# Performance work log

Measured on AMD Instinct MI355X. Metric: run time of the kernel, lower is better.

The kernel has to match this reference:

```python
import jax, jax.numpy as jnp
import numpy as np

B, S, D, H, HD, F = 2, 2048, 2048, 16, 128, 8192
EPS = 1e-5
THETA = 10000.0
NEG = -1e30


def _rmsnorm(x, w):
    v = jnp.mean(jnp.square(x.astype(jnp.float32)), axis=-1, keepdims=True)
    return (x.astype(jnp.float32) * jax.lax.rsqrt(v + EPS)).astype(x.dtype) * w


def _rope(x):
    # x: [B, S, H, HD]; llama-style rotate-half rotary embedding
    inv_freq = 1.0 / (THETA ** (jnp.arange(0, HD, 2, dtype=jnp.float32) / HD))
    ang = jnp.arange(S, dtype=jnp.float32)[:, None] * inv_freq[None, :]  # [S, HD//2]
    cos = jnp.concatenate([jnp.cos(ang), jnp.cos(ang)], axis=-1)[None, :, None, :]
    sin = jnp.concatenate([jnp.sin(ang), jnp.sin(ang)], axis=-1)[None, :, None, :]
    x1, x2 = jnp.split(x, 2, axis=-1)
    return x * cos + jnp.concatenate([-x2, x1], axis=-1) * sin


def _mlp(x, wg, wu, wd):
    # SiLU-gated HiggsAudioMLP: down(silu(gate(x)) * up(x))
    return (jax.nn.silu(x @ wg) * (x @ wu)) @ wd


def setup_inputs() -> dict:
    key = jax.random.key(0)
    ks = jax.random.split(key, 12)
    std = 0.02
    p = lambda k, shape: jax.random.normal(k, shape, dtype=jnp.float32) * std
    return {
        "hidden_states": jax.random.normal(ks[0], (B, S, D), dtype=jnp.float32),
        "audio_out_mask": jax.random.randint(ks[1], (B, S), 0, 2).astype(bool),
        "wq": p(ks[2], (D, H * HD)),
        "wk": p(ks[3], (D, H * HD)),
        "wv": p(ks[4], (D, H * HD)),
        "wo": p(ks[5], (H * HD, D)),
        "input_ln_w": jnp.ones((D,), jnp.float32),
        "post_ln_w": jnp.ones((D,), jnp.float32),
        "audio_post_ln_w": jnp.ones((D,), jnp.float32),
        "w_gate_t": p(ks[6], (D, F)),
        "w_up_t": p(ks[7], (D, F)),
        "w_down_t": p(ks[8], (F, D)),
        "w_gate_a": p(ks[9], (D, F)),
        "w_up_a": p(ks[10], (D, F)),
        "w_down_a": p(ks[11], (F, D)),
    }


def reference(hidden_states, audio_out_mask, wq, wk, wv, wo, input_ln_w, post_ln_w,
              audio_post_ln_w, w_gate_t, w_up_t, w_down_t, w_gate_a, w_up_a, w_down_a):
    # ---- self-attention block ----
    residual = hidden_states
    h = _rmsnorm(hidden_states, input_ln_w)
    q = _rope((h @ wq).reshape(B, S, H, HD))
    k = _rope((h @ wk).reshape(B, S, H, HD))
    v = (h @ wv).reshape(B, S, H, HD)
    scores = jnp.einsum("bqhd,bkhd->bhqk", q, k) / float(np.sqrt(HD))
    causal = jnp.tril(jnp.ones((S, S), bool))
    scores = jnp.where(causal[None, None], scores, NEG)
    attn = jax.nn.softmax(scores, axis=-1)
    ctx = jnp.einsum("bhqk,bkhd->bqhd", attn, v).reshape(B, S, H * HD)
    hidden_states = residual + ctx @ wo
    # ---- dual FFN, per-token routed by audio_out_mask ----
    residual = hidden_states
    text_out = _mlp(_rmsnorm(hidden_states, post_ln_w), w_gate_t, w_up_t, w_down_t)
    audio_out = _mlp(_rmsnorm(hidden_states, audio_post_ln_w), w_gate_a, w_up_a, w_down_a)
    return residual + jnp.where(audio_out_mask[..., None], audio_out, text_out)
```

## Files before the change

### kernel.cpp

```cpp
#include <hip/hip_runtime.h>


#define BB 2
#define SS 2048
#define DD 2048
#define HH 16
#define HDD 128
#define FF 8192
#define TT (BB*SS)
#define RPAD 4608

typedef unsigned short ushort_t;
typedef __bf16 bf16x8 __attribute__((ext_vector_type(8)));
typedef float f32x4 __attribute__((ext_vector_type(4)));

#define DEV static __device__ __forceinline__

DEV float bf2f(ushort_t u) { __bf16 b; __builtin_memcpy(&b, &u, 2); return (float)b; }
DEV ushort_t f2bf(float f) { __bf16 b = (__bf16)f; ushort_t u; __builtin_memcpy(&u, &b, 2); return u; }

DEV void gl_lds16(const ushort_t* g, ushort_t* l) {
    __builtin_amdgcn_global_load_lds((const __attribute__((address_space(1))) void*)g,
                                     (__attribute__((address_space(3))) void*)l, 16, 0, 0);
}

#define BARRIER() do { asm volatile("" ::: "memory"); __builtin_amdgcn_s_barrier(); asm volatile("" ::: "memory"); } while (0)
#define LGKM0()   asm volatile("s_waitcnt lgkmcnt(0)" ::: "memory")

__global__ __launch_bounds__(256) void partition_k(const unsigned char* __restrict__ raw,
                                                   int* __restrict__ perm,
                                                   int* __restrict__ header) {
    __shared__ int flag;
    __shared__ int ct[256], ca[256], st[256], sa[256];
    __shared__ int Nt_s, Na_s;
    const int tid = threadIdx.x;
    if (tid == 0) flag = 0;
    __syncthreads();
    int any = 0;
    for (int i = tid; i < TT; i += 256)
        if ((i & 3) != 0 && raw[i] != 0) any = 1;
    if (any) atomicOr(&flag, 1);
    __syncthreads();
    const int is_byte = flag;
    auto mget = [&](int r) -> int {
        return is_byte ? (raw[r] != 0) : (((const int*)raw)[r] != 0);
    };
    int c0 = 0, c1 = 0;
#pragma unroll
    for (int i = 0; i < 16; ++i) {
        if (mget(tid * 16 + i)) c1++; else c0++;
    }
    ct[tid] = c0; ca[tid] = c1;
    __syncthreads();
    if (tid == 0) {
        int at = 0, aa = 0;
        for (int i = 0; i < 256; ++i) {
            st[i] = at; at += ct[i];
            sa[i] = aa; aa += ca[i];
        }
        Nt_s = at; Na_s = aa;
    }
    __syncthreads();
    const int Nt = Nt_s, Na = Na_s;
    const int A0 = (Nt + 255) & ~255;
    const int live = A0 + ((Na + 255) & ~255);
    int pt = st[tid], pa = A0 + sa[tid];
#pragma unroll
    for (int i = 0; i < 16; ++i) {
        const int r = tid * 16 + i;
        if (mget(r)) perm[pa++] = r; else perm[pt++] = r;
    }
    for (int i = Nt + tid; i < A0; i += 256) perm[i] = -1;
    for (int i = A0 + Na + tid; i < RPAD; i += 256) perm[i] = -1;
    if (tid == 0) { header[0] = Nt; header[1] = A0; header[2] = Na; header[3] = live; }
}

struct ConvSeg { const float* in; ushort_t* out; int K, N, cumEnd; };
struct ConvArgs { ConvSeg s[10]; };

__global__ __launch_bounds__(256) void convw_all(ConvArgs a) {
    __shared__ float t[32][33];
    int bid = blockIdx.x;
    int i = 0;
    while (bid >= a.s[i].cumEnd) ++i;
    const int base = (i == 0) ? 0 : a.s[i - 1].cumEnd;
    const int local = bid - base;
    const float* __restrict__ in = a.s[i].in;
    ushort_t* __restrict__ out = a.s[i].out;
    const int K = a.s[i].K, N = a.s[i].N;
    const int ntile = N >> 5;
    const int n0 = (local % ntile) * 32, k0 = (local / ntile) * 32;
    const int tx = threadIdx.x & 31, ty = threadIdx.x >> 5;
#pragma unroll
    for (int j = 0; j < 4; ++j)
        t[ty + 8 * j][tx] = in[(size_t)(k0 + ty + 8 * j) * N + n0 + tx];
    __syncthreads();
#pragma unroll
    for (int j = 0; j < 4; ++j)
        out[(size_t)(n0 + ty + 8 * j) * K + k0 + tx] = f2bf(t[tx][ty + 8 * j]);
}

__global__ __launch_bounds__(256) void rmsnorm_k(const float* __restrict__ x,
                                                 const float* __restrict__ wt,
                                                 ushort_t* __restrict__ out) {
    const int row = blockIdx.x, tid = threadIdx.x;
    const float4* xr = (const float4*)(x + (size_t)row * DD);
    float4 v0 = xr[tid * 2], v1 = xr[tid * 2 + 1];
    float ss = v0.x * v0.x + v0.y * v0.y + v0.z * v0.z + v0.w * v0.w
             + v1.x * v1.x + v1.y * v1.y + v1.z * v1.z + v1.w * v1.w;
#pragma unroll
    for (int d = 1; d < 64; d <<= 1) ss += __shfl_xor(ss, d);
    __shared__ float red[4];
    if ((tid & 63) == 0) red[tid >> 6] = ss;
    __syncthreads();
    const float tot = red[0] + red[1] + red[2] + red[3];
    const float sc = rsqrtf(tot * (1.0f / DD) + 1e-5f);
    const float4* wr = (const float4*)wt;
    float4 w0 = wr[tid * 2], w1 = wr[tid * 2 + 1];
    ushort_t* o = out + (size_t)row * DD + tid * 8;
    o[0] = f2bf(v0.x * sc * w0.x); o[1] = f2bf(v0.y * sc * w0.y);
    o[2] = f2bf(v0.z * sc * w0.z); o[3] = f2bf(v0.w * sc * w0.w);
    o[4] = f2bf(v1.x * sc * w1.x); o[5] = f2bf(v1.y * sc * w1.y);
    o[6] = f2bf(v1.z * sc * w1.z); o[7] = f2bf(v1.w * sc * w1.w);
}

__global__ __launch_bounds__(256) void rmsnorm_gather(const float* __restrict__ x,
                                                      const float* __restrict__ wt_text,
                                                      const float* __restrict__ wt_audio,
                                                      const int* __restrict__ perm,
                                                      const int* __restrict__ header,
                                                      ushort_t* __restrict__ out) {
    const int i = blockIdx.x, tid = threadIdx.x;
    const int p = perm[i];
    ushort_t* o = out + (size_t)i * DD + tid * 8;
    if (p < 0) {
#pragma unroll
        for (int j = 0; j < 8; ++j) o[j] = 0;
        return;
    }
    const float* wt = (i < header[1]) ? wt_text : wt_audio;
    const float4* xr = (const float4*)(x + (size_t)p * DD);
    float4 v0 = xr[tid * 2], v1 = xr[tid * 2 + 1];
    float ss = v0.x * v0.x + v0.y * v0.y + v0.z * v0.z + v0.w * v0.w
             + v1.x * v1.x + v1.y * v1.y + v1.z * v1.z + v1.w * v1.w;
#pragma unroll
    for (int d = 1; d < 64; d <<= 1) ss += __shfl_xor(ss, d);
    __shared__ float red[4];
    if ((tid & 63) == 0) red[tid >> 6] = ss;
    __syncthreads();
    const float tot = red[0] + red[1] + red[2] + red[3];
    const float sc = rsqrtf(tot * (1.0f / DD) + 1e-5f);
    const float4* wr = (const float4*)wt;
    float4 w0 = wr[tid * 2], w1 = wr[tid * 2 + 1];
    o[0] = f2bf(v0.x * sc * w0.x); o[1] = f2bf(v0.y * sc * w0.y);
    o[2] = f2bf(v0.z * sc * w0.z); o[3] = f2bf(v0.w * sc * w0.w);
    o[4] = f2bf(v1.x * sc * w1.x); o[5] = f2bf(v1.y * sc * w1.y);
    o[6] = f2bf(v1.z * sc * w1.z); o[7] = f2bf(v1.w * sc * w1.w);
}

__global__ __launch_bounds__(256) void rope_tab(float* __restrict__ cosb,
                                                float* __restrict__ sinb) {
    const int idx = blockIdx.x * 256 + threadIdx.x;
    const int s = idx >> 6, i = idx & 63;
    const float inv = powf(10000.0f, -(float)i * (1.0f / 64.0f));
    const float ang = (float)s * inv;
    cosb[idx] = cosf(ang);
    sinb[idx] = sinf(ang);
}

__global__ __launch_bounds__(256) void rope_qk(ushort_t* __restrict__ qb,
                                               ushort_t* __restrict__ kb,
                                               const float* __restrict__ cosb,
                                               const float* __restrict__ sinb) {
    const int gid = blockIdx.x * 256 + threadIdx.x;
    ushort_t* x = (gid < TT * 1024) ? qb : kb;
    const int g = gid & (TT * 1024 - 1);
    const int row = g >> 10, p = g & 1023;
    const int h = p >> 6, d = p & 63;
    const int s = row & (SS - 1);
    const size_t base = (size_t)row * DD + h * HDD + d;
    const float x1 = bf2f(x[base]), x2 = bf2f(x[base + 64]);
    const float c = cosb[s * 64 + d], sn = sinb[s * 64 + d];
    x[base]      = f2bf(x1 * c - x2 * sn);
    x[base + 64] = f2bf(x2 * c + x1 * sn);
}

__global__ __launch_bounds__(256, 2) void gemm_qkv(
    const ushort_t* __restrict__ A, const ushort_t* __restrict__ W,
    ushort_t* __restrict__ qb, ushort_t* __restrict__ kb, ushort_t* __restrict__ vt) {
    __shared__ ushort_t As[128 * 32];
    __shared__ ushort_t Bs[128 * 32];
    const int tid = threadIdx.x;
    const int w = tid >> 6, lane = tid & 63;
    const int bx = blockIdx.x;
    const int kind = bx >> 4;
    const int n0 = (bx & 15) * 128;
    const int m0 = blockIdx.y * 128;
    const int wr = w >> 1, wc = w & 1;
    f32x4 acc[4][4] = {};
    const ushort_t* gA = A + (size_t)m0 * DD;
    const ushort_t* gB = W + (size_t)kind * DD * DD + (size_t)n0 * DD;
    const int c0 = tid, c1 = 256 + tid;
    const int r0 = c0 >> 2, o0 = (c0 & 3) * 8;
    const int r1 = c1 >> 2, o1 = (c1 & 3) * 8;
    ushort_t* lA0 = &As[(w * 64) * 8];
    ushort_t* lA1 = &As[(256 + w * 64) * 8];
    ushort_t* lB0 = &Bs[(w * 64) * 8];
    ushort_t* lB1 = &Bs[(256 + w * 64) * 8];
    for (int k0 = 0; k0 < DD; k0 += 32) {
        __syncthreads();
        gl_lds16(gA + (size_t)r0 * DD + k0 + o0, lA0);
        gl_lds16(gA + (size_t)r1 * DD + k0 + o1, lA1);
        gl_lds16(gB + (size_t)r0 * DD + k0 + o0, lB0);
        gl_lds16(gB + (size_t)r1 * DD + k0 + o1, lB1);
        asm volatile("s_waitcnt vmcnt(0)" ::: "memory");
        __syncthreads();
        const int ko = (lane >> 4) * 8;
        const int ra = wr * 64 + (lane & 15);
        const int rb = wc * 64 + (lane & 15);
        bf16x8 af[4], bfv[4];
#pragma unroll
        for (int mi = 0; mi < 4; ++mi) af[mi] = *(const bf16x8*)&As[(ra + mi * 16) * 32 + ko];
#pragma unroll
        for (int ni = 0; ni < 4; ++ni) bfv[ni] = *(const bf16x8*)&Bs[(rb + ni * 16) * 32 + ko];
#pragma unroll
        for (int mi = 0; mi < 4; ++mi)
#pragma unroll
            for (int ni = 0; ni < 4; ++ni)
                acc[mi][ni] = __builtin_amdgcn_mfma_f32_16x16x32_bf16(af[mi], bfv[ni], acc[mi][ni], 0, 0, 0);
    }
    const int cl = lane & 15, r4 = (lane >> 4) * 4;
#pragma unroll
    for (int mi = 0; mi < 4; ++mi)
#pragma unroll
        for (int ni = 0; ni < 4; ++ni)
#pragma unroll
            for (int j = 0; j < 4; ++j) {
                const int r = m0 + wr * 64 + mi * 16 + r4 + j;
                const int c = n0 + wc * 64 + ni * 16 + cl;
                const ushort_t v = f2bf(acc[mi][ni][j]);
                if (kind == 0) {
                    qb[(size_t)r * DD + c] = v;
                } else if (kind == 1) {
                    kb[(size_t)r * DD + c] = v;
                } else {
                    const int b = r >> 11, s = r & (SS - 1), h = c >> 7, d = c & 127;
                    vt[(((size_t)(b * HH + h) * HDD + d) << 11) + s] = v;
                }
            }
}

__global__ __launch_bounds__(256, 2) void gemm_wo(
    const ushort_t* __restrict__ A, const ushort_t* __restrict__ Bt,
    float* __restrict__ C, const float* __restrict__ resid) {
    __shared__ ushort_t As[128 * 32];
    __shared__ ushort_t Bs[128 * 32];
    const int tid = threadIdx.x;
    const int w = tid >> 6, lane = tid & 63;
    const int m0 = blockIdx.y * 128, n0 = blockIdx.x * 128;
    const int wr = w >> 1, wc = w & 1;
    f32x4 acc[4][4] = {};
    const ushort_t* gA = A + (size_t)m0 * DD;
    const ushort_t* gB = Bt + (size_t)n0 * DD;
    const int c0 = tid, c1 = 256 + tid;
    const int r0 = c0 >> 2, o0 = (c0 & 3) * 8;
    const int r1 = c1 >> 2, o1 = (c1 & 3) * 8;
    ushort_t* lA0 = &As[(w * 64) * 8];
    ushort_t* lA1 = &As[(256 + w * 64) * 8];
    ushort_t* lB0 = &Bs[(w * 64) * 8];
    ushort_t* lB1 = &Bs[(256 + w * 64) * 8];
    for (int k0 = 0; k0 < DD; k0 += 32) {
        __syncthreads();
        gl_lds16(gA + (size_t)r0 * DD + k0 + o0, lA0);
        gl_lds16(gA + (size_t)r1 * DD + k0 + o1, lA1);
        gl_lds16(gB + (size_t)r0 * DD + k0 + o0, lB0);
        gl_lds16(gB + (size_t)r1 * DD + k0 + o1, lB1);
        asm volatile("s_waitcnt vmcnt(0)" ::: "memory");
        __syncthreads();
        const int ko = (lane >> 4) * 8;
        const int ra = wr * 64 + (lane & 15);
        const int rb = wc * 64 + (lane & 15);
        bf16x8 af[4], bfv[4];
#pragma unroll
        for (int mi = 0; mi < 4; ++mi) af[mi] = *(const bf16x8*)&As[(ra + mi * 16) * 32 + ko];
#pragma unroll
        for (int ni = 0; ni < 4; ++ni) bfv[ni] = *(const bf16x8*)&Bs[(rb + ni * 16) * 32 + ko];
#pragma unroll
        for (int mi = 0; mi < 4; ++mi)
#pragma unroll
            for (int ni = 0; ni < 4; ++ni)
                acc[mi][ni] = __builtin_amdgcn_mfma_f32_16x16x32_bf16(af[mi], bfv[ni], acc[mi][ni], 0, 0, 0);
    }
    const int cl = lane & 15, r4 = (lane >> 4) * 4;
#pragma unroll
    for (int mi = 0; mi < 4; ++mi)
#pragma unroll
        for (int ni = 0; ni < 4; ++ni)
#pragma unroll
            for (int j = 0; j < 4; ++j) {
                const int r = m0 + wr * 64 + mi * 16 + r4 + j;
                const int c = n0 + wc * 64 + ni * 16 + cl;
                const size_t idx = (size_t)r * DD + c;
                C[idx] = resid[idx] + acc[mi][ni][j];
            }
}

__global__ __launch_bounds__(256, 2) void gemm_down_c(
    const ushort_t* __restrict__ A, const ushort_t* __restrict__ Bt_text,
    const ushort_t* __restrict__ Bt_audio, float* __restrict__ C,
    const int* __restrict__ perm, const int* __restrict__ header) {
    const int m0 = blockIdx.y * 128;
    if (m0 >= header[3]) return;
    const ushort_t* Bt = (m0 >= header[1]) ? Bt_audio : Bt_text;
    __shared__ ushort_t As[128 * 32];
    __shared__ ushort_t Bs[128 * 32];
    const int tid = threadIdx.x;
    const int w = tid >> 6, lane = tid & 63;
    const int n0 = blockIdx.x * 128;
    const int wr = w >> 1, wc = w & 1;
    f32x4 acc[4][4] = {};
    const ushort_t* gA = A + (size_t)m0 * FF;
    const ushort_t* gB = Bt + (size_t)n0 * FF;
    const int c0 = tid, c1 = 256 + tid;
    const int r0 = c0 >> 2, o0 = (c0 & 3) * 8;
    const int r1 = c1 >> 2, o1 = (c1 & 3) * 8;
    ushort_t* lA0 = &As[(w * 64) * 8];
    ushort_t* lA1 = &As[(256 + w * 64) * 8];
    ushort_t* lB0 = &Bs[(w * 64) * 8];
    ushort_t* lB1 = &Bs[(256 + w * 64) * 8];
    for (int k0 = 0; k0 < FF; k0 += 32) {
        __syncthreads();
        gl_lds16(gA + (size_t)r0 * FF + k0 + o0, lA0);
        gl_lds16(gA + (size_t)r1 * FF + k0 + o1, lA1);
        gl_lds16(gB + (size_t)r0 * FF + k0 + o0, lB0);
        gl_lds16(gB + (size_t)r1 * FF + k0 + o1, lB1);
        asm volatile("s_waitcnt vmcnt(0)" ::: "memory");
        __syncthreads();
        const int ko = (lane >> 4) * 8;
        const int ra = wr * 64 + (lane & 15);
        const int rb = wc * 64 + (lane & 15);
        bf16x8 af[4], bfv[4];
#pragma unroll
        for (int mi = 0; mi < 4; ++mi) af[mi] = *(const bf16x8*)&As[(ra + mi * 16) * 32 + ko];
#pragma unroll
        for (int ni = 0; ni < 4; ++ni) bfv[ni] = *(const bf16x8*)&Bs[(rb + ni * 16) * 32 + ko];
#pragma unroll
        for (int mi = 0; mi < 4; ++mi)
#pragma unroll
            for (int ni = 0; ni < 4; ++ni)
                acc[mi][ni] = __builtin_amdgcn_mfma_f32_16x16x32_bf16(af[mi], bfv[ni], acc[mi][ni], 0, 0, 0);
    }
    const int cl = lane & 15, r4 = (lane >> 4) * 4;
#pragma unroll
    for (int mi = 0; mi < 4; ++mi)
#pragma unroll
        for (int ni = 0; ni < 4; ++ni)
#pragma unroll
            for (int j = 0; j < 4; ++j) {
                const int r = m0 + wr * 64 + mi * 16 + r4 + j;
                const int p = perm[r];
                if (p >= 0) {
                    const int c = n0 + wc * 64 + ni * 16 + cl;
                    float* q = C + (size_t)p * DD + c;
                    *q = *q + acc[mi][ni][j];
                }
            }
}

__global__ __launch_bounds__(512, 2) void gemm_gu8(
    const ushort_t* __restrict__ A,
    const ushort_t* __restrict__ Bg_t, const ushort_t* __restrict__ Bu_t,
    const ushort_t* __restrict__ Bg_a, const ushort_t* __restrict__ Bu_a,
    ushort_t* __restrict__ act, const int* __restrict__ header) {
    const int nwg = gridDim.x * gridDim.y;
    int bid = blockIdx.y * gridDim.x + blockIdx.x;
    bid = (bid & 7) * (nwg >> 3) + (bid >> 3);
    const int bx = bid % 64;
    const int by = bid / 64;
    const int m0 = by * 256;
    if (m0 >= header[3]) return;
    const bool audio = (m0 >= header[1]);
    const ushort_t* Bg = audio ? Bg_a : Bg_t;
    const ushort_t* Bu = audio ? Bu_a : Bu_t;
    const int n0g = bx * 128;

    __shared__ ushort_t smem[65536];
    const int tid = threadIdx.x;
    const int w = tid >> 6, lane = tid & 63;
    const int wm = w >> 2, wn = w & 3;
    const int f16 = lane & 15, g4 = lane >> 4;

    const int rl = tid >> 3;
    const int cc8 = (((tid & 7) ^ ((tid >> 3) & 7)) * 8);
    const int wchunk = w * 64;

    const ushort_t* gA = A + (size_t)m0 * DD;

    auto stageA_h = [&](int buf, int k0, int h) {
#pragma unroll
        for (int j = 0; j < 2; ++j) {
            const int r = h * 128 + j * 64 + rl;
            gl_lds16(gA + (size_t)r * DD + k0 + cc8,
                     &smem[buf * 32768 + h * 8192 + (j * 512 + wchunk) * 8]);
        }
    };
    auto stageB_h = [&](int buf, int k0, int h) {
#pragma unroll
        for (int j = 0; j < 2; ++j) {
            const int br = h * 128 + j * 64 + rl;
            const int ty = (br >> 4) & 1;
            const int grow = ((br >> 5) << 4) + (br & 15);
            const ushort_t* src = (ty ? Bu : Bg) + (size_t)(n0g + grow) * DD + k0 + cc8;
            gl_lds16(src, &smem[buf * 32768 + 16384 + h * 8192 + (j * 512 + wchunk) * 8]);
        }
    };

    const int aBase = (wm * 128 + f16) * 64;
    const int bBase = (wn * 64 + f16) * 64;
    int cswz[2];
    cswz[0] = ((g4 ^ (f16 & 7)) * 8);
    cswz[1] = (((4 + g4) ^ (f16 & 7)) * 8);

    f32x4 acc[8][4] = {};
    bf16x8 af[4][2], b0[2][2], b1[2][2];

    stageA_h(0, 0, 0); stageA_h(0, 0, 1);
    stageB_h(0, 0, 0); stageB_h(0, 0, 1);
    stageA_h(1, 64, 0); stageB_h(1, 64, 0);
    asm volatile("s_waitcnt vmcnt(4)" ::: "memory");
    BARRIER();

    const int nt = DD / 64;
    for (int t = 0; t < nt; ++t) {
        const int buf = t & 1, obuf = buf ^ 1;
        const int ab = buf * 32768, bb = buf * 32768 + 16384;
        const int k1 = (t + 1) * 64, k2 = (t + 2) * 64;
        const bool pf1 = (t + 1) < nt, pf2 = (t + 2) < nt;
#pragma unroll
        for (int m = 0; m < 4; ++m)
#pragma unroll
            for (int ks = 0; ks < 2; ++ks)
                af[m][ks] = *(const bf16x8*)&smem[ab + aBase + m * 1024 + cswz[ks]];
#pragma unroll
        for (int n = 0; n < 2; ++n)
#pragma unroll
            for (int ks = 0; ks < 2; ++ks)
                b0[n][ks] = *(const bf16x8*)&smem[bb + bBase + n * 1024 + cswz[ks]];
        if (pf1) stageA_h(obuf, k1, 1);
        BARRIER();
        LGKM0();
        __builtin_amdgcn_s_setprio(1);
#pragma unroll
        for (int m = 0; m < 4; ++m)
#pragma unroll
            for (int n = 0; n < 2; ++n)
#pragma unroll
                for (int ks = 0; ks < 2; ++ks)
                    acc[m][n] = __builtin_amdgcn_mfma_f32_16x16x32_bf16(af[m][ks], b0[n][ks], acc[m][n], 0, 0, 0);
        __builtin_amdgcn_s_setprio(0);
        BARRIER();
#pragma unroll
        for (int n = 0; n < 2; ++n)
#pragma unroll
            for (int ks = 0; ks < 2; ++ks)
                b1[n][ks] = *(const bf16x8*)&smem[bb + bBase + (2 + n) * 1024 + cswz[ks]];
        if (pf1) stageB_h(obuf, k1, 1);
        BARRIER();
        LGKM0();
        __builtin_amdgcn_s_setprio(1);
#pragma unroll
        for (int m = 0; m < 4; ++m)
#pragma unroll
            for (int n = 0; n < 2; ++n)
#pragma unroll
                for (int ks = 0; ks < 2; ++ks)
                    acc[m][2 + n] = __builtin_amdgcn_mfma_f32_16x16x32_bf16(af[m][ks], b1[n][ks], acc[m][2 + n], 0, 0, 0);
        __builtin_amdgcn_s_setprio(0);
        BARRIER();
#pragma unroll
        for (int m = 0; m < 4; ++m)
#pragma unroll
            for (int ks = 0; ks < 2; ++ks)
                af[m][ks] = *(const bf16x8*)&smem[ab + aBase + (4 + m) * 1024 + cswz[ks]];
        BARRIER();
        LGKM0();
        __builtin_amdgcn_s_setprio(1);
#pragma unroll
        for (int m = 0; m < 4; ++m)
#pragma unroll
            for (int n = 0; n < 2; ++n)
#pragma unroll
                for (int ks = 0; ks < 2; ++ks)
                    acc[4 + m][n] = __builtin_amdgcn_mfma_f32_16x16x32_bf16(af[m][ks], b0[n][ks], acc[4 + m][n], 0, 0, 0);
        __builtin_amdgcn_s_setprio(0);
        BARRIER();
        if (pf2) { stageA_h(buf, k2, 0); stageB_h(buf, k2, 0); }
        BARRIER();
        __builtin_amdgcn_s_setprio(1);
#pragma unroll
        for (int m = 0; m < 4; ++m)
#pragma unroll
            for (int n = 0; n < 2; ++n)
#pragma unroll
                for (int ks = 0; ks < 2; ++ks)
                    acc[4 + m][2 + n] = __builtin_amdgcn_mfma_f32_16x16x32_bf16(af[m][ks], b1[n][ks], acc[4 + m][2 + n], 0, 0, 0);
        __builtin_amdgcn_s_setprio(0);
        if (pf2)      { asm volatile("s_waitcnt vmcnt(4)" ::: "memory"); }
        else if (pf1) { asm volatile("s_waitcnt vmcnt(0)" ::: "memory"); }
        BARRIER();
    }

    const int r4 = g4 * 4;
#pragma unroll
    for (int m = 0; m < 8; ++m)
#pragma unroll
        for (int np = 0; np < 2; ++np) {
            const int f = n0g + (wn * 2 + np) * 16 + f16;
#pragma unroll
            for (int j = 0; j < 4; ++j) {
                const int r = m0 + wm * 128 + m * 16 + r4 + j;
                const float g = acc[m][np * 2][j], u = acc[m][np * 2 + 1][j];
                act[(size_t)r * FF + f] = f2bf(g / (1.0f + __expf(-g)) * u);
            }
        }
}

__global__ __launch_bounds__(512, 2) void attn_k(
    const ushort_t* __restrict__ qb, const ushort_t* __restrict__ kb,
    const ushort_t* __restrict__ vt, ushort_t* __restrict__ ctx) {
    __shared__ ushort_t Ks[2][64 * 128];
    __shared__ ushort_t Vs[2][128 * 64];
    __shared__ ushort_t Pw[8][16 * 64];
    const int tid = threadIdx.x, w = tid >> 6, lane = tid & 63;
    const int qt = gridDim.x - 1 - blockIdx.x;
    const int bh = blockIdx.y, b = bh >> 4, h = bh & 15;
    const int q0 = qt * 128 + w * 16;
    const int f16 = lane & 15, g4 = lane >> 4;
    bf16x8 aq[4];
    {
        const ushort_t* qr = qb + ((size_t)(b * SS + q0 + f16)) * DD + h * HDD + g4 * 8;
#pragma unroll
        for (int ko = 0; ko < 4; ++ko) aq[ko] = *(const bf16x8*)(qr + ko * 32);
    }
    auto stageKV = [&](int bufi, int kt) {
        const int sk0 = kt * 64;
#pragma unroll
        for (int i = 0; i < 2; ++i) {
            const int c = i * 512 + tid;
            const int csrc = ((c & 15) ^ ((c >> 4) & 7)) * 8;
            gl_lds16(kb + ((size_t)(b * SS + sk0 + (c >> 4))) * DD + h * HDD + csrc,
                     &Ks[bufi][(i * 512 + w * 64) * 8]);
        }
#pragma unroll
        for (int i = 0; i < 2; ++i) {
            const int c = i * 512 + tid;
            const int csrc = ((c & 7) ^ ((c >> 3) & 7)) * 8;
            gl_lds16(vt + ((size_t)((b * HH + h) * HDD + (c >> 3))) * SS + sk0 + csrc,
                     &Vs[bufi][(i * 512 + w * 64) * 8]);
        }
    };
    f32x4 o[8] = {};
    float mrow[4] = {-3e38f, -3e38f, -3e38f, -3e38f};
    float lrow[4] = {};
    const int nkv = 2 * qt + 2;
    stageKV(0, 0);
    for (int kt = 0; kt < nkv; ++kt) {
        const int cur = kt & 1;
        if (kt < nkv - 1) {
            stageKV(cur ^ 1, kt + 1);
            asm volatile("s_waitcnt vmcnt(4)" ::: "memory");
        } else {
            asm volatile("s_waitcnt vmcnt(0)" ::: "memory");
        }
        BARRIER();
        f32x4 s[4] = {};
#pragma unroll
        for (int ko = 0; ko < 4; ++ko)
#pragma unroll
            for (int ni = 0; ni < 4; ++ni) {
                bf16x8 bk = *(const bf16x8*)&Ks[cur][(ni * 16 + f16) * 128 + (((ko * 4 + g4) ^ (f16 & 7)) * 8)];
                s[ni] = __builtin_amdgcn_mfma_f32_16x16x32_bf16(aq[ko], bk, s[ni], 0, 0, 0);
            }
        const float scale = 0.08838834764831843f;
#pragma unroll
        for (int ni = 0; ni < 4; ++ni)
#pragma unroll
            for (int j = 0; j < 4; ++j) {
                float v = s[ni][j] * scale;
                const int kg = kt * 64 + ni * 16 + f16;
                const int qg = q0 + g4 * 4 + j;
                if (kg > qg) v = -1e30f;
                s[ni][j] = v;
            }
#pragma unroll
        for (int j = 0; j < 4; ++j) {
            float tm = fmaxf(fmaxf(s[0][j], s[1][j]), fmaxf(s[2][j], s[3][j]));
#pragma unroll
            for (int dd = 1; dd < 16; dd <<= 1) tm = fmaxf(tm, __shfl_xor(tm, dd));
            const float mn = fmaxf(mrow[j], tm);
            const float corr = __expf(mrow[j] - mn);
            float sum = 0.f;
#pragma unroll
            for (int ni = 0; ni < 4; ++ni) {
                const float p = __expf(s[ni][j] - mn);
                s[ni][j] = p;
                sum += p;
            }
#pragma unroll
            for (int dd = 1; dd < 16; dd <<= 1) sum += __shfl_xor(sum, dd);
            lrow[j] = lrow[j] * corr + sum;
            mrow[j] = mn;
#pragma unroll
            for (int di = 0; di < 8; ++di) o[di][j] *= corr;
        }
#pragma unroll
        for (int ni = 0; ni < 4; ++ni)
#pragma unroll
            for (int j = 0; j < 4; ++j) {
                const int prow = g4 * 4 + j;
                const int pcb = ni * 2 + (f16 >> 3);
                Pw[w][prow * 64 + ((pcb ^ (prow & 7)) * 8) + (f16 & 7)] = f2bf(s[ni][j]);
            }
#pragma unroll
        for (int ks = 0; ks < 2; ++ks) {
            bf16x8 pa = *(const bf16x8*)&Pw[w][f16 * 64 + (((ks * 4 + g4) ^ (f16 & 7)) * 8)];
#pragma unroll
            for (int di = 0; di < 8; ++di) {
                bf16x8 bv = *(const bf16x8*)&Vs[cur][(di * 16 + f16) * 64 + (((ks * 4 + g4) ^ (f16 & 7)) * 8)];
                o[di] = __builtin_amdgcn_mfma_f32_16x16x32_bf16(pa, bv, o[di], 0, 0, 0);
            }
        }
        BARRIER();
    }
    float inv[4];
#pragma unroll
    for (int j = 0; j < 4; ++j) inv[j] = 1.0f / lrow[j];
#pragma unroll
    for (int di = 0; di < 8; ++di)
#pragma unroll
        for (int j = 0; j < 4; ++j) {
            const int r = q0 + g4 * 4 + j;
            ctx[((size_t)(b * SS + r)) * DD + h * HDD + di * 16 + f16] = f2bf(o[di][j] * inv[j]);
        }
}

extern "C" void kernel_launch(void* const* d_in, const int* in_sizes, int n_in,
                              void* d_out, int out_size, void* d_ws, size_t ws_size,
                              hipStream_t stream) {
    (void)in_sizes; (void)n_in; (void)out_size; (void)ws_size;
    const float* hs  = (const float*)d_in[0];
    const unsigned char* mask_raw = (const unsigned char*)d_in[1];
    const float* wq  = (const float*)d_in[2];
    const float* wk  = (const float*)d_in[3];
    const float* wv  = (const float*)d_in[4];
    const float* wo  = (const float*)d_in[5];
    const float* iln = (const float*)d_in[6];
    const float* pln = (const float*)d_in[7];
    const float* aln = (const float*)d_in[8];
    const float* wgt = (const float*)d_in[9];
    const float* wut = (const float*)d_in[10];
    const float* wdt = (const float*)d_in[11];
    const float* wga = (const float*)d_in[12];
    const float* wua = (const float*)d_in[13];
    const float* wda = (const float*)d_in[14];

    const size_t SZ_W1 = (size_t)DD * DD * 2;
    const size_t SZ_W2 = (size_t)DD * FF * 2;
    const size_t SZ_A  = (size_t)TT * DD * 2;

    char* ws = (char*)d_ws;
    size_t off = 0;
    auto take = [&](size_t n) { char* p = ws + off; off += n; return p; };
    ushort_t* wq_t  = (ushort_t*)take(SZ_W1);
    ushort_t* wk_t  = (ushort_t*)take(SZ_W1);
    ushort_t* wv_t  = (ushort_t*)take(SZ_W1);
    ushort_t* wo_t  = (ushort_t*)take(SZ_W1);
    ushort_t* wg_tb = (ushort_t*)take(SZ_W2);
    ushort_t* wu_tb = (ushort_t*)take(SZ_W2);
    ushort_t* wd_tb = (ushort_t*)take(SZ_W2);
    ushort_t* wg_ab = (ushort_t*)take(SZ_W2);
    ushort_t* wu_ab = (ushort_t*)take(SZ_W2);
    ushort_t* wd_ab = (ushort_t*)take(SZ_W2);
    char* actreg = take(6 * SZ_A);
    float* cosb = (float*)take((size_t)SS * 64 * 4);
    float* sinb = (float*)take((size_t)SS * 64 * 4);
    int* perm   = (int*)take(RPAD * 4);
    int* header = (int*)take(64);

    ushort_t* h_bf = (ushort_t*)(actreg);
    ushort_t* qb   = (ushort_t*)(actreg + 1 * SZ_A);
    ushort_t* kb   = (ushort_t*)(actreg + 2 * SZ_A);
    ushort_t* vt   = (ushort_t*)(actreg + 3 * SZ_A);
    ushort_t* ctx  = (ushort_t*)(actreg + 4 * SZ_A);
    ushort_t* hn_c  = (ushort_t*)(actreg);
    ushort_t* act_c = (ushort_t*)(actreg + (size_t)RPAD * DD * 2);

    const dim3 blk(256);

    partition_k<<<1, blk, 0, stream>>>(mask_raw, perm, header);

    ConvArgs ca;
    int cum = 0;
    auto seg = [&](int i, const float* in, ushort_t* out, int K, int N) {
        cum += (N / 32) * (K / 32);
        ca.s[i] = ConvSeg{in, out, K, N, cum};
    };
    seg(0, wq, wq_t, DD, DD);
    seg(1, wk, wk_t, DD, DD);
    seg(2, wv, wv_t, DD, DD);
    seg(3, wo, wo_t, DD, DD);
    seg(4, wgt, wg_tb, DD, FF);
    seg(5, wut, wu_tb, DD, FF);
    seg(6, wdt, wd_tb, FF, DD);
    seg(7, wga, wg_ab, DD, FF);
    seg(8, wua, wu_ab, DD, FF);
    seg(9, wda, wd_ab, FF, DD);
    convw_all<<<cum, blk, 0, stream>>>(ca);

    rope_tab<<<(SS * 64) / 256, blk, 0, stream>>>(cosb, sinb);

    rmsnorm_k<<<TT, blk, 0, stream>>>(hs, iln, h_bf);
    gemm_qkv<<<dim3(48, TT / 128), blk, 0, stream>>>(h_bf, wq_t, qb, kb, vt);
    rope_qk<<<(2 * TT * 1024) / 256, blk, 0, stream>>>(qb, kb, cosb, sinb);
    attn_k<<<dim3(SS / 128, BB * HH), dim3(512), 0, stream>>>(qb, kb, vt, ctx);
    gemm_wo<<<dim3(DD / 128, TT / 128), blk, 0, stream>>>(ctx, wo_t, (float*)d_out, hs);

    rmsnorm_gather<<<RPAD, blk, 0, stream>>>((const float*)d_out, pln, aln, perm, header, hn_c);
    gemm_gu8<<<dim3(FF / 128, RPAD / 256), dim3(512), 0, stream>>>(hn_c, wg_tb, wu_tb, wg_ab, wu_ab, act_c, header);
    gemm_down_c<<<dim3(DD / 128, RPAD / 128), blk, 0, stream>>>(act_c, wd_tb, wd_ab, (float*)d_out, perm, header);
}
```

Baseline: 1.110 ms.

## Replace QKV and output GEMMs with pipelined 256x128 template kernel; lazy softmax rescale

Replaces the simple single-buffered gemm_qkv and gemm_wo kernels with one templated 512-thread kernel. It uses 256x128 tiles, K-step 64, a double-buffered LDS with XOR swizzle, staggered global-to-LDS loads overlapped with MFMA, s_setprio around the MFMA phases, and a block-id remap across XCDs. This targets the per-iteration full vmcnt(0) stalls and the low data reuse of the old kernels. Separately, the attention softmax now skips the running-max rescale of the output accumulators unless the new max exceeds the old one by more than 8 anywhere in the wave. That saves exp and multiply work, but lets exponentials grow up to e^8 before renormalising.

```diff
diff --git a/kernel.cpp b/kernel.cpp
--- a/kernel.cpp
+++ b/kernel.cpp
@@ -185,123 +185,140 @@
     x[base + 64] = f2bf(x2 * c + x1 * sn);
 }
 
-__global__ __launch_bounds__(256, 2) void gemm_qkv(
+template <int EPI>
+__global__ __launch_bounds__(512, 2) void gemm_nt8(
     const ushort_t* __restrict__ A, const ushort_t* __restrict__ W,
-    ushort_t* __restrict__ qb, ushort_t* __restrict__ kb, ushort_t* __restrict__ vt) {
-    __shared__ ushort_t As[128 * 32];
-    __shared__ ushort_t Bs[128 * 32];
+    int K, ushort_t* __restrict__ o0, ushort_t* __restrict__ o1,
+    ushort_t* __restrict__ o2, float* __restrict__ Cf,
+    const float* __restrict__ resid) {
+    const int nwg = gridDim.x * gridDim.y;
+    int bid = blockIdx.y * gridDim.x + blockIdx.x;
+    bid = (bid & 7) * (nwg >> 3) + (bid >> 3);
+    const int bxx = bid % gridDim.x;
+    const int byy = bid / gridDim.x;
+    const int m0 = byy * 256;
+    int kind = 0, n0;
+    const ushort_t* B;
+    if (EPI == 0) {
+        kind = bxx >> 4;
+        n0 = (bxx & 15) * 128;
+        B = W + (size_t)kind * DD * DD + (size_t)n0 * K;
+    } else {
+        n0 = bxx * 128;
+        B = W + (size_t)n0 * K;
+    }
+    __shared__ ushort_t smem[49152];
     const int tid = threadIdx.x;
     const int w = tid >> 6, lane = tid & 63;
-    const int bx = blockIdx.x;
-    const int kind = bx >> 4;
-    const int n0 = (bx & 15) * 128;
-    const int m0 = blockIdx.y * 128;
-    const int wr = w >> 1, wc = w & 1;
-    f32x4 acc[4][4] = {};
-    const ushort_t* gA = A + (size_t)m0 * DD;
-    const ushort_t* gB = W + (size_t)kind * DD * DD + (size_t)n0 * DD;
-    const int c0 = tid, c1 = 256 + tid;
-    const int r0 = c0 >> 2, o0 = (c0 & 3) * 8;
-    const int r1 = c1 >> 2, o1 = (c1 & 3) * 8;
-    ushort_t* lA0 = &As[(w * 64) * 8];
-    ushort_t* lA1 = &As[(256 + w * 64) * 8];
-    ushort_t* lB0 = &Bs[(w * 64) * 8];
-    ushort_t* lB1 = &Bs[(256 + w * 64) * 8];
-    for (int k0 = 0; k0 < DD; k0 += 32) {
-        __syncthreads();
-        gl_lds16(gA + (size_t)r0 * DD + k0 + o0, lA0);
-        gl_lds16(gA + (size_t)r1 * DD + k0 + o1, lA1);
-        gl_lds16(gB + (size_t)r0 * DD + k0 + o0, lB0);
-        gl_lds16(gB + (size_t)r1 * DD + k0 + o1, lB1);
-        asm volatile("s_waitcnt vmcnt(0)" ::: "memory");
-        __syncthreads();
-        const int ko = (lane >> 4) * 8;
-        const int ra = wr * 64 + (lane & 15);
-        const int rb = wc * 64 + (lane & 15);
-        bf16x8 af[4], bfv[4];
-#pragma unroll
-        for (int mi = 0; mi < 4; ++mi) af[mi] = *(const bf16x8*)&As[(ra + mi * 16) * 32 + ko];
-#pragma unroll
-        for (int ni = 0; ni < 4; ++ni) bfv[ni] = *(const bf16x8*)&Bs[(rb + ni * 16) * 32 + ko];
-#pragma unroll
-        for (int mi = 0; mi < 4; ++mi)
-#pragma unroll
-            for (int ni = 0; ni < 4; ++ni)
-                acc[mi][ni] = __builtin_amdgcn_mfma_f32_16x16x32_bf16(af[mi], bfv[ni], acc[mi][ni], 0, 0, 0);
-    }
-    const int cl = lane & 15, r4 = (lane >> 4) * 4;
-#pragma unroll
-    for (int mi = 0; mi < 4; ++mi)
-#pragma unroll
-        for (int ni = 0; ni < 4; ++ni)
+    const int wm = w >> 2, wn = w & 3;
+    const int f16 = lane & 15, g4 = lane >> 4;
+    const int rl = tid >> 3;
+    const int cc8 = (((tid & 7) ^ ((tid >> 3) & 7)) * 8);
+    const ushort_t* gA = A + (size_t)m0 * K;
+
+    auto stageAq = [&](int buf, int k0, int q) {
+        gl_lds16(gA + (size_t)(q * 64 + rl) * K + k0 + cc8,
+                 &smem[buf * 24576 + q * 4096 + w * 512]);
+    };
+    auto stageB2 = [&](int buf, int k0) {
+#pragma unroll
+        for (int j = 0; j < 2; ++j)
+            gl_lds16(B + (size_t)(j * 64 + rl) * K + k0 + cc8,
+                     &smem[buf * 24576 + 16384 + j * 4096 + w * 512]);
+    };
+
+    const int aBase = (wm * 128 + f16) * 64;
+    const int bBase = (wn * 32 + f16) * 64;
+    int cswz[2];
+    cswz[0] = ((g4 ^ (f16 & 7)) * 8);
+    cswz[1] = (((4 + g4) ^ (f16 & 7)) * 8);
+
+    f32x4 acc[8][2] = {};
+    bf16x8 af[4][2], bfr[2][2];
+
+    stageAq(0, 0, 0); stageAq(0, 0, 1); stageAq(0, 0, 2); stageAq(0, 0, 3);
+    stageB2(0, 0);
+    stageAq(1, 64, 0); stageAq(1, 64, 2); stageB2(1, 64);
+    asm volatile("s_waitcnt vmcnt(4)" ::: "memory");
+    BARRIER();
+
+    const int nt = K / 64;
+    for (int t = 0; t < nt; ++t) {
+        const int cur = t & 1;
+        const int ab = cur * 24576, bb = cur * 24576 + 16384;
+#pragma unroll
+        for (int m = 0; m < 4; ++m)
+#pragma unroll
+            for (int ks = 0; ks < 2; ++ks)
+                af[m][ks] = *(const bf16x8*)&smem[ab + aBase + m * 1024 + cswz[ks]];
+#pragma unroll
+        for (int np = 0; np < 2; ++np)
+#pragma unroll
+            for (int ks = 0; ks < 2; ++ks)
+                bfr[np][ks] = *(const bf16x8*)&smem[bb + bBase + np * 1024 + cswz[ks]];
+        if (t + 1 < nt) {
+            stageAq(1 - cur, (t + 1) * 64, 1);
+            stageAq(1 - cur, (t + 1) * 64, 3);
+        }
+        BARRIER();
+        LGKM0();
+        __builtin_amdgcn_s_setprio(1);
+#pragma unroll
+        for (int m = 0; m < 4; ++m)
+#pragma unroll
+            for (int np = 0; np < 2; ++np)
+#pragma unroll
+                for (int ks = 0; ks < 2; ++ks)
+                    acc[m][np] = __builtin_amdgcn_mfma_f32_16x16x32_bf16(af[m][ks], bfr[np][ks], acc[m][np], 0, 0, 0);
+        __builtin_amdgcn_s_setprio(0);
+        BARRIER();
+#pragma unroll
+        for (int m = 0; m < 4; ++m)
+#pragma unroll
+            for (int ks = 0; ks < 2; ++ks)
+                af[m][ks] = *(const bf16x8*)&smem[ab + aBase + (4 + m) * 1024 + cswz[ks]];
+        if (t + 2 < nt) {
+            stageAq(cur, (t + 2) * 64, 0);
+            stageAq(cur, (t + 2) * 64, 2);
+            stageB2(cur, (t + 2) * 64);
+        }
+        BARRIER();
+        LGKM0();
+        __builtin_amdgcn_s_setprio(1);
+#pragma unroll
+        for (int m = 0; m < 4; ++m)
+#pragma unroll
+            for (int np = 0; np < 2; ++np)
+#pragma unroll
+                for (int ks = 0; ks < 2; ++ks)
+                    acc[4 + m][np] = __builtin_amdgcn_mfma_f32_16x16x32_bf16(af[m][ks], bfr[np][ks], acc[4 + m][np], 0, 0, 0);
+        __builtin_amdgcn_s_setprio(0);
+        if (t + 2 < nt) { asm volatile("s_waitcnt vmcnt(4)" ::: "memory"); }
+        else            { asm volatile("s_waitcnt vmcnt(0)" ::: "memory"); }
+        BARRIER();
+    }
+
+#pragma unroll
+    for (int m = 0; m < 8; ++m)
+#pragma unroll
+        for (int np = 0; np < 2; ++np)
 #pragma unroll
             for (int j = 0; j < 4; ++j) {
-                const int r = m0 + wr * 64 + mi * 16 + r4 + j;
-                const int c = n0 + wc * 64 + ni * 16 + cl;
-                const ushort_t v = f2bf(acc[mi][ni][j]);
-                if (kind == 0) {
-                    qb[(size_t)r * DD + c] = v;
-                } else if (kind == 1) {
-                    kb[(size_t)r * DD + c] = v;
+                const int r = m0 + wm * 128 + m * 16 + g4 * 4 + j;
+                const int c = n0 + wn * 32 + np * 16 + f16;
+                const float v = acc[m][np][j];
+                if (EPI == 0) {
+                    const ushort_t vb = f2bf(v);
+                    if (kind == 0)      o0[(size_t)r * DD + c] = vb;
+                    else if (kind == 1) o1[(size_t)r * DD + c] = vb;
+                    else {
+                        const int b = r >> 11, s = r & (SS - 1), h = c >> 7, d = c & 127;
+                        o2[(((size_t)(b * HH + h) * HDD + d) << 11) + s] = vb;
+                    }
                 } else {
-                    const int b = r >> 11, s = r & (SS - 1), h = c >> 7, d = c & 127;
-                    vt[(((size_t)(b * HH + h) * HDD + d) << 11) + s] = v;
+                    const size_t idx = (size_t)r * DD + c;
+                    Cf[idx] = resid[idx] + v;
                 }
-            }
-}
-
-__global__ __launch_bounds__(256, 2) void gemm_wo(
-    const ushort_t* __restrict__ A, const ushort_t* __restrict__ Bt,
-    float* __restrict__ C, const float* __restrict__ resid) {
-    __shared__ ushort_t As[128 * 32];
-    __shared__ ushort_t Bs[128 * 32];
-    const int tid = threadIdx.x;
-    const int w = tid >> 6, lane = tid & 63;
-    const int m0 = blockIdx.y * 128, n0 = blockIdx.x * 128;
-    const int wr = w >> 1, wc = w & 1;
-    f32x4 acc[4][4] = {};
-    const ushort_t* gA = A + (size_t)m0 * DD;
-    const ushort_t* gB = Bt + (size_t)n0 * DD;
-    const int c0 = tid, c1 = 256 + tid;
-    const int r0 = c0 >> 2, o0 = (c0 & 3) * 8;
-    const int r1 = c1 >> 2, o1 = (c1 & 3) * 8;
-    ushort_t* lA0 = &As[(w * 64) * 8];
-    ushort_t* lA1 = &As[(256 + w * 64) * 8];
-    ushort_t* lB0 = &Bs[(w * 64) * 8];
-    ushort_t* lB1 = &Bs[(256 + w * 64) * 8];
-    for (int k0 = 0; k0 < DD; k0 += 32) {
-        __syncthreads();
-        gl_lds16(gA + (size_t)r0 * DD + k0 + o0, lA0);
-        gl_lds16(gA + (size_t)r1 * DD + k0 + o1, lA1);
-        gl_lds16(gB + (size_t)r0 * DD + k0 + o0, lB0);
-        gl_lds16(gB + (size_t)r1 * DD + k0 + o1, lB1);
-        asm volatile("s_waitcnt vmcnt(0)" ::: "memory");
-        __syncthreads();
-        const int ko = (lane >> 4) * 8;
-        const int ra = wr * 64 + (lane & 15);
-        const int rb = wc * 64 + (lane & 15);
-        bf16x8 af[4], bfv[4];
-#pragma unroll
-        for (int mi = 0; mi < 4; ++mi) af[mi] = *(const bf16x8*)&As[(ra + mi * 16) * 32 + ko];
-#pragma unroll
-        for (int ni = 0; ni < 4; ++ni) bfv[ni] = *(const bf16x8*)&Bs[(rb + ni * 16) * 32 + ko];
-#pragma unroll
-        for (int mi = 0; mi < 4; ++mi)
-#pragma unroll
-            for (int ni = 0; ni < 4; ++ni)
-                acc[mi][ni] = __builtin_amdgcn_mfma_f32_16x16x32_bf16(af[mi], bfv[ni], acc[mi][ni], 0, 0, 0);
-    }
-    const int cl = lane & 15, r4 = (lane >> 4) * 4;
-#pragma unroll
-    for (int mi = 0; mi < 4; ++mi)
-#pragma unroll
-        for (int ni = 0; ni < 4; ++ni)
-#pragma unroll
-            for (int j = 0; j < 4; ++j) {
-                const int r = m0 + wr * 64 + mi * 16 + r4 + j;
-                const int c = n0 + wc * 64 + ni * 16 + cl;
-                const size_t idx = (size_t)r * DD + c;
-                C[idx] = resid[idx] + acc[mi][ni][j];
             }
 }
 
@@ -597,21 +614,24 @@
             float tm = fmaxf(fmaxf(s[0][j], s[1][j]), fmaxf(s[2][j], s[3][j]));
 #pragma unroll
             for (int dd = 1; dd < 16; dd <<= 1) tm = fmaxf(tm, __shfl_xor(tm, dd));
-            const float mn = fmaxf(mrow[j], tm);
-            const float corr = __expf(mrow[j] - mn);
+            if (!__all(tm <= mrow[j] + 8.0f)) {
+                const float mn = fmaxf(mrow[j], tm);
+                const float corr = __expf(mrow[j] - mn);
+                lrow[j] *= corr;
+#pragma unroll
+                for (int di = 0; di < 8; ++di) o[di][j] *= corr;
+                mrow[j] = mn;
+            }
             float sum = 0.f;
 #pragma unroll
             for (int ni = 0; ni < 4; ++ni) {
-                const float p = __expf(s[ni][j] - mn);
+                const float p = __expf(s[ni][j] - mrow[j]);
                 s[ni][j] = p;
                 sum += p;
             }
 #pragma unroll
             for (int dd = 1; dd < 16; dd <<= 1) sum += __shfl_xor(sum, dd);
-            lrow[j] = lrow[j] * corr + sum;
-            mrow[j] = mn;
-#pragma unroll
-            for (int di = 0; di < 8; ++di) o[di][j] *= corr;
+            lrow[j] += sum;
         }
 #pragma unroll
         for (int ni = 0; ni < 4; ++ni)
@@ -720,10 +740,12 @@
     rope_tab<<<(SS * 64) / 256, blk, 0, stream>>>(cosb, sinb);
 
     rmsnorm_k<<<TT, blk, 0, stream>>>(hs, iln, h_bf);
-    gemm_qkv<<<dim3(48, TT / 128), blk, 0, stream>>>(h_bf, wq_t, qb, kb, vt);
+    gemm_nt8<0><<<dim3(48, TT / 256), dim3(512), 0, stream>>>(
+        h_bf, wq_t, DD, qb, kb, vt, nullptr, nullptr);
     rope_qk<<<(2 * TT * 1024) / 256, blk, 0, stream>>>(qb, kb, cosb, sinb);
     attn_k<<<dim3(SS / 128, BB * HH), dim3(512), 0, stream>>>(qb, kb, vt, ctx);
-    gemm_wo<<<dim3(DD / 128, TT / 128), blk, 0, stream>>>(ctx, wo_t, (float*)d_out, hs);
+    gemm_nt8<1><<<dim3(DD / 128, TT / 256), dim3(512), 0, stream>>>(
+        ctx, wo_t, DD, nullptr, nullptr, nullptr, (float*)d_out, hs);
 
     rmsnorm_gather<<<RPAD, blk, 0, stream>>>((const float*)d_out, pln, aln, perm, header, hn_c);
     gemm_gu8<<<dim3(FF / 128, RPAD / 256), dim3(512), 0, stream>>>(hn_c, wg_tb, wu_tb, wg_ab, wu_ab, act_c, header);
```

New measurement: 1.103 ms. About the same (-0.7%).
